# Performance work log

Hardware: AMD Instinct MI355X
Metric: run time of the kernel (lower is better)

Reference implementation:

```python
import jax, jax.numpy as jnp
import numpy as np

N_NODES = 50000
N_EDGES = 800000
NUM_FEATURES = 128
HIDDEN = 64
ODE_STEPS = 32  # fixed-step dopri5 (deterministic stand-in for adaptive dopri5)


def gcn_conv(h, edge_index, W, b):
    """PyG GCNConv: add self-loops, symmetric deg^-1/2 normalization, linear."""
    n = h.shape[0]
    hw = h @ W  # [N, out]
    loops = jnp.arange(n, dtype=edge_index.dtype)
    src = jnp.concatenate([edge_index[0], loops])
    dst = jnp.concatenate([edge_index[1], loops])
    deg = jax.ops.segment_sum(jnp.ones_like(src, dtype=hw.dtype), dst, num_segments=n)
    dinv = jnp.where(deg > 0, jax.lax.rsqrt(deg), 0.0)
    coef = dinv[src] * dinv[dst]  # [E+N]
    msg = hw[src] * coef[:, None]
    out = jax.ops.segment_sum(msg, dst, num_segments=n)
    return out + b


def dopri5_fixed(f, y0, t0, t1, n_steps):
    """Fixed-step Dormand-Prince RK45 from t0 to t1 (autonomous-friendly)."""
    h = (t1 - t0) / n_steps
    A = [
        (1 / 5,),
        (3 / 40, 9 / 40),
        (44 / 45, -56 / 15, 32 / 9),
        (19372 / 6561, -25360 / 2187, 64448 / 6561, -212 / 729),
        (9017 / 3168, -355 / 33, 46732 / 5247, 49 / 176, -5103 / 18656),
        (35 / 384, 0.0, 500 / 1113, 125 / 192, -2187 / 6784, 11 / 84),
    ]
    C = (0.0, 1 / 5, 3 / 10, 4 / 5, 8 / 9, 1.0)
    B = (35 / 384, 0.0, 500 / 1113, 125 / 192, -2187 / 6784, 11 / 84, 0.0)

    def step(y, i):
        t = t0 + h * i.astype(y.dtype)
        ks = [f(t, y)]
        for row, c in zip(A, C[1:]):
            yi = y + h * sum(a * k for a, k in zip(row, ks))
            ks.append(f(t + c * h, yi))
        y_next = y + h * sum(b * k for b, k in zip(B, ks) if b != 0.0)
        return y_next, None

    y, _ = jax.lax.scan(step, y0, jnp.arange(n_steps))
    return y


def setup_inputs() -> dict:
    key = jax.random.key(0)
    ks = jax.random.split(key, 12)
    s = 1.0 / np.sqrt(NUM_FEATURES)
    sh = 1.0 / np.sqrt(HIDDEN)
    s2 = 1.0 / np.sqrt(2 * HIDDEN)
    return {
        "x": jax.random.normal(ks[0], (N_NODES, NUM_FEATURES), jnp.float32),
        "pos_edge_index": jax.random.randint(ks[1], (2, N_EDGES), 0, N_NODES, jnp.int64),
        "neg_edge_index": jax.random.randint(ks[2], (2, N_EDGES), 0, N_NODES, jnp.int64),
        "t": jnp.array([0.0, 1.0], jnp.float32),
        "W_enc": jax.random.uniform(ks[3], (NUM_FEATURES, HIDDEN), jnp.float32, -s, s),
        "b_enc": jax.random.uniform(ks[4], (HIDDEN,), jnp.float32, -s, s),
        "W_pos": jax.random.uniform(ks[5], (HIDDEN, HIDDEN), jnp.float32, -sh, sh),
        "b_pos": jax.random.uniform(ks[6], (HIDDEN,), jnp.float32, -sh, sh),
        "W_neg": jax.random.uniform(ks[7], (HIDDEN, HIDDEN), jnp.float32, -sh, sh),
        "b_neg": jax.random.uniform(ks[8], (HIDDEN,), jnp.float32, -sh, sh),
        "W_ode": jax.random.uniform(ks[9], (2 * HIDDEN, 2 * HIDDEN), jnp.float32, -s2, s2),
        "b_ode": jax.random.uniform(ks[10], (2 * HIDDEN,), jnp.float32, -s2, s2),
    }


def reference(x, pos_edge_index, neg_edge_index, t, W_enc, b_enc, W_pos, b_pos,
              W_neg, b_neg, W_ode, b_ode):
    h = x @ W_enc + b_enc  # feature_encoder
    h_pos = gcn_conv(h, pos_edge_index, W_pos, b_pos)
    h_neg = gcn_conv(h, neg_edge_index, W_neg, b_neg)
    h = jnp.concatenate([h_pos, h_neg], axis=1)  # [N, 2*hidden]

    def ode_f(_t, y):
        return jnp.tanh(y @ W_ode + b_ode)

    return dopri5_fixed(ode_f, h, t[0], t[1], ODE_STEPS)
```

## Files before the change

kernel.cpp:

```cpp
#include <hip/hip_runtime.h>
#include <hip/hip_bf16.h>


typedef __attribute__((ext_vector_type(8))) short short8v;
typedef __attribute__((ext_vector_type(4))) float f32x4;
typedef __attribute__((ext_vector_type(2))) unsigned uint2v;

__device__ __forceinline__ float fast_tanh(float x) {
    float e = __builtin_amdgcn_exp2f(x * 2.8853900817779268f);
    return 1.0f - 2.0f * __builtin_amdgcn_rcpf(e + 1.0f);
}

__device__ __forceinline__ unsigned bf16r(float x) {
    unsigned u = __float_as_uint(x);
    return (u + 0x7fffu + ((u >> 16) & 1u)) >> 16;
}
__device__ __forceinline__ unsigned cvt_pk(float lo, float hi) {
    unsigned r;
    asm("v_cvt_pk_bf16_f32 %0, %1, %2" : "=v"(r) : "v"(lo), "v"(hi));
    return r;
}


__global__ __launch_bounds__(256) void deg_init_kernel(float* degp, float* degn, int n) {
    int i = blockIdx.x * 256 + threadIdx.x;
    if (i < n) { degp[i] = 1.0f; degn[i] = 1.0f; }
}

__global__ __launch_bounds__(256) void deg_count_kernel(const int* __restrict__ pdst,
        const int* __restrict__ ndst, float* degp, float* degn, int nE) {
    int e = blockIdx.x * 256 + threadIdx.x;
    if (e < nE) {
        atomicAdd(&degp[pdst[e]], 1.0f);
        atomicAdd(&degn[ndst[e]], 1.0f);
    }
}

__global__ __launch_bounds__(256) void dinv_kernel(float* degp, float* degn, int n) {
    int i = blockIdx.x * 256 + threadIdx.x;
    if (i < n) { degp[i] = rsqrtf(degp[i]); degn[i] = rsqrtf(degn[i]); }
}


__global__ __launch_bounds__(256) void encoder_kernel(const float* __restrict__ x,
        const float* __restrict__ W, const float* __restrict__ b,
        float* __restrict__ h, int n) {
    __shared__ __align__(16) float Ws[128 * 64];
    __shared__ __align__(16) float xs[4 * 128];
    int tid = threadIdx.x;
    for (int i = tid; i < 128 * 64; i += 256) Ws[i] = W[i];
    long row = (long)blockIdx.x * 4;
    for (int i = tid; i < 4 * 128; i += 256) {
        long rr = row + (i >> 7);
        xs[i] = (rr < n) ? x[rr * 128 + (i & 127)] : 0.0f;
    }
    __syncthreads();
    int r = tid >> 6, c = tid & 63;
    float acc = b[c];
    #pragma unroll 8
    for (int k = 0; k < 128; k += 4) {
        float4 xv = *(const float4*)&xs[r * 128 + k];
        acc += xv.x * Ws[(k+0)*64+c] + xv.y * Ws[(k+1)*64+c]
             + xv.z * Ws[(k+2)*64+c] + xv.w * Ws[(k+3)*64+c];
    }
    if (row + r < n) h[(row + r) * 64 + c] = acc;
}


__global__ __launch_bounds__(256) void hw_kernel(const float* __restrict__ h,
        const float* __restrict__ Wp, const float* __restrict__ Wn,
        const float* __restrict__ dinvp, const float* __restrict__ dinvn,
        float* __restrict__ hwp, float* __restrict__ hwn, int n) {
    __shared__ __align__(16) float Wps[64 * 64];
    __shared__ __align__(16) float Wns[64 * 64];
    __shared__ __align__(16) float hs[4 * 64];
    int tid = threadIdx.x;
    for (int i = tid; i < 64 * 64; i += 256) { Wps[i] = Wp[i]; Wns[i] = Wn[i]; }
    long row = (long)blockIdx.x * 4;
    {
        int i = tid;
        long rr = row + (i >> 6);
        hs[i] = (rr < n) ? h[rr * 64 + (i & 63)] : 0.0f;
    }
    __syncthreads();
    int r = tid >> 6, c = tid & 63;
    float ap = 0.0f, an = 0.0f;
    #pragma unroll 4
    for (int k = 0; k < 64; k += 4) {
        float4 hv = *(const float4*)&hs[r * 64 + k];
        ap += hv.x*Wps[(k+0)*64+c] + hv.y*Wps[(k+1)*64+c] + hv.z*Wps[(k+2)*64+c] + hv.w*Wps[(k+3)*64+c];
        an += hv.x*Wns[(k+0)*64+c] + hv.y*Wns[(k+1)*64+c] + hv.z*Wns[(k+2)*64+c] + hv.w*Wns[(k+3)*64+c];
    }
    if (row + r < n) {
        hwp[(row + r) * 64 + c] = ap * dinvp[row + r];
        hwn[(row + r) * 64 + c] = an * dinvn[row + r];
    }
}


__global__ __launch_bounds__(256) void y0_init_kernel(const float* __restrict__ hwp,
        const float* __restrict__ hwn, float* __restrict__ y0, int n) {
    long idx = (long)blockIdx.x * 256 + threadIdx.x;
    if (idx >= (long)n * 128) return;
    long i = idx >> 7; int c = (int)(idx & 127);
    y0[idx] = (c < 64) ? hwp[i * 64 + c] : hwn[i * 64 + (c - 64)];
}

__global__ __launch_bounds__(256) void scatter_kernel(const int* __restrict__ src,
        const int* __restrict__ dst, const float* __restrict__ hw,
        float* __restrict__ y0, int colOff, int nE) {
    int wid  = blockIdx.x * 4 + (threadIdx.x >> 6);
    int lane = threadIdx.x & 63;
    if (wid >= nE) return;
    int s = src[wid], d = dst[wid];
    atomicAdd(&y0[(long)d * 128 + colOff + lane], hw[(long)s * 64 + lane]);
}

__global__ __launch_bounds__(256) void finalize_kernel(float* __restrict__ y0,
        const float* __restrict__ dinvp, const float* __restrict__ dinvn,
        const float* __restrict__ bp, const float* __restrict__ bn, int n) {
    long idx = (long)blockIdx.x * 256 + threadIdx.x;
    if (idx >= (long)n * 128) return;
    long i = idx >> 7; int c = (int)(idx & 127);
    if (c < 64) y0[idx] = dinvp[i] * y0[idx] + bp[c];
    else        y0[idx] = dinvn[i] * y0[idx] + bn[c - 64];
}


#define MFMA_(A, B, C) __builtin_amdgcn_mfma_f32_16x16x32_bf16(A, B, C, 0, 0, 0)

#define ODE_STAGE(BUF, YIM, CONSM) {                                                \
    char* yr_ = (BUF) + rowoff;                                                     \
    uint2v pk_;                                                                     \
    pk_.x = cvt_pk(YIM(0,0), YIM(0,1)); pk_.y = cvt_pk(YIM(0,2), YIM(0,3));         \
    *(uint2v*)(yr_ + (g0off ^ swz)) = pk_;                                          \
    pk_.x = cvt_pk(YIM(1,0), YIM(1,1)); pk_.y = cvt_pk(YIM(1,2), YIM(1,3));         \
    *(uint2v*)(yr_ + (g1off ^ swz)) = pk_;                                          \
    __syncthreads();                                                                \
    short8v b0 = *(const short8v*)(yr_ + ((  0 + q16) ^ swz));                      \
    short8v b1 = *(const short8v*)(yr_ + (( 64 + q16) ^ swz));                      \
    short8v b2 = *(const short8v*)(yr_ + ((128 + q16) ^ swz));                      \
    short8v b3 = *(const short8v*)(yr_ + ((192 + q16) ^ swz));                      \
    {                                                                               \
        f32x4 a = bias0;                                                            \
        a = MFMA_(af00, b0, a); a = MFMA_(af01, b1, a);                             \
        a = MFMA_(af02, b2, a); a = MFMA_(af03, b3, a);                             \
        CONSM(0, fast_tanh(a[0]), fast_tanh(a[1]), fast_tanh(a[2]), fast_tanh(a[3])); \
    }                                                                               \
    {                                                                               \
        f32x4 a = bias1;                                                            \
        a = MFMA_(af10, b0, a); a = MFMA_(af11, b1, a);                             \
        a = MFMA_(af12, b2, a); a = MFMA_(af13, b3, a);                             \
        CONSM(1, fast_tanh(a[0]), fast_tanh(a[1]), fast_tanh(a[2]), fast_tanh(a[3])); \
    } }

#define YI1(nn, r) (y[nn][r])
#define YI2(nn, r) (y[nn][r] + c21 * kp1[nn][r])
#define YI3(nn, r) (y[nn][r] + c31 * kp1[nn][r] + c32 * kp2[nn][r])
#define YI4(nn, r) (y[nn][r] + c41 * kp1[nn][r] + c42 * kp2[nn][r] + c43 * kp3[nn][r])
#define YI5(nn, r) (y[nn][r] + c51 * kp1[nn][r] + c52 * kp2[nn][r] + c53 * kp3[nn][r] \
                             + c54 * kp4[nn][r])
#define YI6(nn, r) (y[nn][r] + c61 * kp1[nn][r] + c62 * kp2[nn][r] + c63 * kp3[nn][r] \
                             + c64 * kp4[nn][r] + c65 * kp5[nn][r])

#define CONS1(nn,t0,t1,t2,t3) { kp1[nn][0]=t0; kp1[nn][1]=t1; kp1[nn][2]=t2; kp1[nn][3]=t3; }
#define CONS2(nn,t0,t1,t2,t3) { kp2[nn][0]=t0; kp2[nn][1]=t1; kp2[nn][2]=t2; kp2[nn][3]=t3; }
#define CONS3(nn,t0,t1,t2,t3) { kp3[nn][0]=t0; kp3[nn][1]=t1; kp3[nn][2]=t2; kp3[nn][3]=t3; }
#define CONS4(nn,t0,t1,t2,t3) { kp4[nn][0]=t0; kp4[nn][1]=t1; kp4[nn][2]=t2; kp4[nn][3]=t3; }
#define CONS5(nn,t0,t1,t2,t3) { kp5[nn][0]=t0; kp5[nn][1]=t1; kp5[nn][2]=t2; kp5[nn][3]=t3; }
#define CONS6(nn,t0,t1,t2,t3) {                                             \
    y[nn][0] += d1 * kp1[nn][0] + d3 * kp3[nn][0] + d4 * kp4[nn][0]         \
              + d5 * kp5[nn][0] + d6 * (t0);                                \
    y[nn][1] += d1 * kp1[nn][1] + d3 * kp3[nn][1] + d4 * kp4[nn][1]         \
              + d5 * kp5[nn][1] + d6 * (t1);                                \
    y[nn][2] += d1 * kp1[nn][2] + d3 * kp3[nn][2] + d4 * kp4[nn][2]         \
              + d5 * kp5[nn][2] + d6 * (t2);                                \
    y[nn][3] += d1 * kp1[nn][3] + d3 * kp3[nn][3] + d4 * kp4[nn][3]         \
              + d5 * kp5[nn][3] + d6 * (t3); }

__global__ __launch_bounds__(256) void ode_mfma_kernel(const float* __restrict__ y0,
        float* __restrict__ out, const float* __restrict__ W,
        const float* __restrict__ bb, const float* __restrict__ tt, int nrows) {
    __shared__ __align__(16) char smem[32768];
    int tid  = threadIdx.x;
    int lane = tid & 63, w = tid >> 6;
    int l15 = lane & 15, q = lane >> 4;
    int swz = (lane & 7) << 4, q16 = q * 16, q8 = q * 8;
    int rowoff = l15 * 256;
    int g0off = w * 64 + q8, g1off = w * 64 + 32 + q8;

    for (int i = tid; i < 16384; i += 256) {
        int d = i >> 7, c = i & 127;
        unsigned short hb = (unsigned short)bf16r(W[i]);
        *(unsigned short*)(smem + c * 256 + ((d * 2) ^ ((c & 7) << 4))) = hb;
    }
    __syncthreads();

    const char* ab0 = smem + ((2 * w) * 16 + l15) * 256;
    const char* ab1 = smem + ((2 * w + 1) * 16 + l15) * 256;
    short8v af00 = *(const short8v*)(ab0 + ((  0 + q16) ^ swz));
    short8v af01 = *(const short8v*)(ab0 + (( 64 + q16) ^ swz));
    short8v af02 = *(const short8v*)(ab0 + ((128 + q16) ^ swz));
    short8v af03 = *(const short8v*)(ab0 + ((192 + q16) ^ swz));
    short8v af10 = *(const short8v*)(ab1 + ((  0 + q16) ^ swz));
    short8v af11 = *(const short8v*)(ab1 + (( 64 + q16) ^ swz));
    short8v af12 = *(const short8v*)(ab1 + ((128 + q16) ^ swz));
    short8v af13 = *(const short8v*)(ab1 + ((192 + q16) ^ swz));
    __syncthreads();

    float hstep = (tt[1] - tt[0]) * 0.03125f;
    float c21 = hstep * 0.2f;
    float c31 = hstep * 0.075f,               c32 = hstep * 0.225f;
    float c41 = hstep * 0.9777777777777777f,  c42 = hstep * -3.7333333333333334f,
          c43 = hstep * 3.5555555555555554f;
    float c51 = hstep * 2.9525986892242035f,  c52 = hstep * -11.595793324188385f,
          c53 = hstep * 9.822892851699436f,   c54 = hstep * -0.2908093278463649f;
    float c61 = hstep * 2.8462752525252526f,  c62 = hstep * -10.757575757575758f,
          c63 = hstep * 8.906422717743473f,   c64 = hstep * 0.2784090909090909f,
          c65 = hstep * -0.2735313036020583f;
    float d1 = hstep * 0.09114583333333333f,  d3 = hstep * 0.44923629829290207f,
          d4 = hstep * 0.6510416666666666f,   d5 = hstep * -0.322376179245283f,
          d6 = hstep * 0.13095238095238096f;

    f32x4 bias0 = *(const f32x4*)&bb[(2 * w)     * 16 + q * 4];
    f32x4 bias1 = *(const f32x4*)&bb[(2 * w + 1) * 16 + q * 4];

    long grow = (long)blockIdx.x * 16 + l15;
    bool ok = grow < nrows;

    f32x4 y[2];
    if (ok) {
        y[0] = *(const f32x4*)&y0[grow * 128 + (2 * w)     * 16 + q * 4];
        y[1] = *(const f32x4*)&y0[grow * 128 + (2 * w + 1) * 16 + q * 4];
    } else {
        y[0] = (f32x4){0.0f, 0.0f, 0.0f, 0.0f};
        y[1] = (f32x4){0.0f, 0.0f, 0.0f, 0.0f};
    }

    char* bufA = smem;
    char* bufB = smem + 4096;

    f32x4 kp1[2], kp2[2], kp3[2], kp4[2], kp5[2];

    #pragma unroll 1
    for (int step = 0; step < 32; ++step) {
        ODE_STAGE(bufA, YI1, CONS1);
        ODE_STAGE(bufB, YI2, CONS2);
        ODE_STAGE(bufA, YI3, CONS3);
        ODE_STAGE(bufB, YI4, CONS4);
        ODE_STAGE(bufA, YI5, CONS5);
        ODE_STAGE(bufB, YI6, CONS6);
    }

    if (ok) {
        *(f32x4*)&out[grow * 128 + (2 * w)     * 16 + q * 4] = y[0];
        *(f32x4*)&out[grow * 128 + (2 * w + 1) * 16 + q * 4] = y[1];
    }
}


extern "C" void kernel_launch(void* const* d_in, const int* in_sizes, int n_in,
                              void* d_out, int out_size, void* d_ws, size_t ws_size,
                              hipStream_t stream) {
    const float* x     = (const float*)d_in[0];
    const int*   pei   = (const int*)d_in[1];
    const int*   nei   = (const int*)d_in[2];
    const float* t     = (const float*)d_in[3];
    const float* W_enc = (const float*)d_in[4];
    const float* b_enc = (const float*)d_in[5];
    const float* W_pos = (const float*)d_in[6];
    const float* b_pos = (const float*)d_in[7];
    const float* W_neg = (const float*)d_in[8];
    const float* b_neg = (const float*)d_in[9];
    const float* W_ode = (const float*)d_in[10];
    const float* b_ode = (const float*)d_in[11];

    int n  = in_sizes[0] / 128;
    int nE = in_sizes[1] / 2;

    float* ws    = (float*)d_ws;
    float* h     = ws;
    float* y0    = ws + (long)n * 64;
    float* dinvp = y0 + (long)n * 128;
    float* dinvn = dinvp + n;

    float* hwp = (float*)d_out;
    float* hwn = hwp + (long)n * 64;

    const int* psrc = pei;       const int* pdst = pei + nE;
    const int* nsrc = nei;       const int* ndst = nei + nE;

    int nbN  = (n + 255) / 256;
    int nbE  = (nE + 255) / 256;
    int nbR  = (n + 3) / 4;
    long tot = (long)n * 128;
    int nbT  = (int)((tot + 255) / 256);

    deg_init_kernel <<<nbN, 256, 0, stream>>>(dinvp, dinvn, n);
    deg_count_kernel<<<nbE, 256, 0, stream>>>(pdst, ndst, dinvp, dinvn, nE);
    dinv_kernel     <<<nbN, 256, 0, stream>>>(dinvp, dinvn, n);
    encoder_kernel  <<<nbR, 256, 0, stream>>>(x, W_enc, b_enc, h, n);
    hw_kernel       <<<nbR, 256, 0, stream>>>(h, W_pos, W_neg, dinvp, dinvn, hwp, hwn, n);
    y0_init_kernel  <<<nbT, 256, 0, stream>>>(hwp, hwn, y0, n);
    scatter_kernel  <<<(nE + 3) / 4, 256, 0, stream>>>(psrc, pdst, hwp, y0, 0,  nE);
    scatter_kernel  <<<(nE + 3) / 4, 256, 0, stream>>>(nsrc, ndst, hwn, y0, 64, nE);
    finalize_kernel <<<nbT, 256, 0, stream>>>(y0, dinvp, dinvn, b_pos, b_neg, n);
    ode_mfma_kernel <<<(n + 15) / 16, 256, 0, stream>>>(y0, (float*)d_out, W_ode, b_ode, t, n);
}
```

Measured before the change: 1.176 ms.

## Replace atomic scatter with CSR build and per-node gather aggregation

Replaces the float atomicAdd scatter of messages into y0 with a CSR build (count, single-block scan, fill) and a gather kernel where one wavefront per destination node sums neighbour rows. The degree normalization, self-loop and bias are folded into the gather, which removes the y0_init and finalize passes. The goal is to avoid roughly 100M float atomics and the extra full passes over y0. In exchange it adds integer atomics for counting and filling, plus a serial-ish 2-block scan over 50k nodes. The workspace formerly used for h is reused for the CSR arrays after hw_kernel has consumed h.

```diff
diff --git a/kernel.cpp b/kernel.cpp
--- a/kernel.cpp
+++ b/kernel.cpp
@@ -19,26 +19,6 @@
     unsigned r;
     asm("v_cvt_pk_bf16_f32 %0, %1, %2" : "=v"(r) : "v"(lo), "v"(hi));
     return r;
-}
-
-
-__global__ __launch_bounds__(256) void deg_init_kernel(float* degp, float* degn, int n) {
-    int i = blockIdx.x * 256 + threadIdx.x;
-    if (i < n) { degp[i] = 1.0f; degn[i] = 1.0f; }
-}
-
-__global__ __launch_bounds__(256) void deg_count_kernel(const int* __restrict__ pdst,
-        const int* __restrict__ ndst, float* degp, float* degn, int nE) {
-    int e = blockIdx.x * 256 + threadIdx.x;
-    if (e < nE) {
-        atomicAdd(&degp[pdst[e]], 1.0f);
-        atomicAdd(&degn[ndst[e]], 1.0f);
-    }
-}
-
-__global__ __launch_bounds__(256) void dinv_kernel(float* degp, float* degn, int n) {
-    int i = blockIdx.x * 256 + threadIdx.x;
-    if (i < n) { degp[i] = rsqrtf(degp[i]); degn[i] = rsqrtf(degn[i]); }
 }
 
 
@@ -69,7 +49,6 @@
 
 __global__ __launch_bounds__(256) void hw_kernel(const float* __restrict__ h,
         const float* __restrict__ Wp, const float* __restrict__ Wn,
-        const float* __restrict__ dinvp, const float* __restrict__ dinvn,
         float* __restrict__ hwp, float* __restrict__ hwn, int n) {
     __shared__ __align__(16) float Wps[64 * 64];
     __shared__ __align__(16) float Wns[64 * 64];
@@ -92,38 +71,114 @@
         an += hv.x*Wns[(k+0)*64+c] + hv.y*Wns[(k+1)*64+c] + hv.z*Wns[(k+2)*64+c] + hv.w*Wns[(k+3)*64+c];
     }
     if (row + r < n) {
-        hwp[(row + r) * 64 + c] = ap * dinvp[row + r];
-        hwn[(row + r) * 64 + c] = an * dinvn[row + r];
-    }
-}
-
-
-__global__ __launch_bounds__(256) void y0_init_kernel(const float* __restrict__ hwp,
-        const float* __restrict__ hwn, float* __restrict__ y0, int n) {
-    long idx = (long)blockIdx.x * 256 + threadIdx.x;
-    if (idx >= (long)n * 128) return;
-    long i = idx >> 7; int c = (int)(idx & 127);
-    y0[idx] = (c < 64) ? hwp[i * 64 + c] : hwn[i * 64 + (c - 64)];
-}
-
-__global__ __launch_bounds__(256) void scatter_kernel(const int* __restrict__ src,
-        const int* __restrict__ dst, const float* __restrict__ hw,
-        float* __restrict__ y0, int colOff, int nE) {
-    int wid  = blockIdx.x * 4 + (threadIdx.x >> 6);
-    int lane = threadIdx.x & 63;
-    if (wid >= nE) return;
-    int s = src[wid], d = dst[wid];
-    atomicAdd(&y0[(long)d * 128 + colOff + lane], hw[(long)s * 64 + lane]);
-}
-
-__global__ __launch_bounds__(256) void finalize_kernel(float* __restrict__ y0,
+        hwp[(row + r) * 64 + c] = ap;
+        hwn[(row + r) * 64 + c] = an;
+    }
+}
+
+
+__global__ __launch_bounds__(256) void cnt_zero_kernel(int* cntp, int* cntn, int n) {
+    int i = blockIdx.x * 256 + threadIdx.x;
+    if (i < n) { cntp[i] = 0; cntn[i] = 0; }
+}
+
+__global__ __launch_bounds__(256) void count_kernel(const int* __restrict__ pdst,
+        const int* __restrict__ ndst, int* cntp, int* cntn, int nE) {
+    int e = blockIdx.x * 256 + threadIdx.x;
+    if (e < nE) {
+        atomicAdd(&cntp[pdst[e]], 1);
+        atomicAdd(&cntn[ndst[e]], 1);
+    }
+}
+
+__global__ __launch_bounds__(1024) void scan_kernel(int* cntp, int* cntn,
+        int* rpp, int* rpn, float* dinvp, float* dinvn, int n) {
+    int* cnt  = blockIdx.x ? cntn  : cntp;
+    int* rp   = blockIdx.x ? rpn   : rpp;
+    float* dv = blockIdx.x ? dinvn : dinvp;
+    __shared__ int ps[1024];
+    int t = threadIdx.x;
+    int CH = (n + 1023) / 1024;
+    int beg = t * CH, end = beg + CH; if (end > n) end = n;
+    int s = 0;
+    for (int i = beg; i < end && i >= 0; ++i) s += cnt[i];
+    ps[t] = s;
+    __syncthreads();
+    for (int off = 1; off < 1024; off <<= 1) {
+        int v = (t >= off) ? ps[t - off] : 0;
+        __syncthreads();
+        ps[t] += v;
+        __syncthreads();
+    }
+    int run = (t == 0) ? 0 : ps[t - 1];
+    for (int i = beg; i < end && i >= 0; ++i) {
+        int c = cnt[i];
+        rp[i] = run; run += c;
+        dv[i] = rsqrtf((float)c + 1.0f);
+        cnt[i] = 0;
+    }
+    if (t == 1023) rp[n] = ps[1023];
+}
+
+__global__ __launch_bounds__(256) void fill_kernel(const int* __restrict__ src,
+        const int* __restrict__ dst, const int* __restrict__ rp,
+        int* cur, int* outarr, int nE) {
+    int e = blockIdx.x * 256 + threadIdx.x;
+    if (e >= nE) return;
+    int d = dst[e];
+    int pos = rp[d] + atomicAdd(&cur[d], 1);
+    outarr[pos] = src[e];
+}
+
+
+__global__ __launch_bounds__(256) void aggregate_kernel(
+        const float* __restrict__ hwp, const float* __restrict__ hwn,
+        const int* __restrict__ srcp, const int* __restrict__ srcn,
+        const int* __restrict__ rpp, const int* __restrict__ rpn,
         const float* __restrict__ dinvp, const float* __restrict__ dinvn,
-        const float* __restrict__ bp, const float* __restrict__ bn, int n) {
-    long idx = (long)blockIdx.x * 256 + threadIdx.x;
-    if (idx >= (long)n * 128) return;
-    long i = idx >> 7; int c = (int)(idx & 127);
-    if (c < 64) y0[idx] = dinvp[i] * y0[idx] + bp[c];
-    else        y0[idx] = dinvn[i] * y0[idx] + bn[c - 64];
+        const float* __restrict__ bp, const float* __restrict__ bn,
+        float* __restrict__ y0, int n) {
+    int w = threadIdx.x >> 6, lane = threadIdx.x & 63;
+    int d = blockIdx.x * 4 + w;
+    if (d >= n) return;
+    {
+        int beg = rpp[d], end = rpp[d + 1];
+        float s0 = 0, s1 = 0, s2 = 0, s3 = 0;
+        int i = beg;
+        for (; i + 4 <= end; i += 4) {
+            int a0 = srcp[i], a1 = srcp[i+1], a2 = srcp[i+2], a3 = srcp[i+3];
+            s0 += dinvp[a0] * hwp[(long)a0 * 64 + lane];
+            s1 += dinvp[a1] * hwp[(long)a1 * 64 + lane];
+            s2 += dinvp[a2] * hwp[(long)a2 * 64 + lane];
+            s3 += dinvp[a3] * hwp[(long)a3 * 64 + lane];
+        }
+        for (; i < end; ++i) {
+            int a0 = srcp[i];
+            s0 += dinvp[a0] * hwp[(long)a0 * 64 + lane];
+        }
+        float dv = dinvp[d];
+        float sum = (s0 + s1) + (s2 + s3) + dv * hwp[(long)d * 64 + lane];
+        y0[(long)d * 128 + lane] = dv * sum + bp[lane];
+    }
+    {
+        int beg = rpn[d], end = rpn[d + 1];
+        float s0 = 0, s1 = 0, s2 = 0, s3 = 0;
+        int i = beg;
+        for (; i + 4 <= end; i += 4) {
+            int a0 = srcn[i], a1 = srcn[i+1], a2 = srcn[i+2], a3 = srcn[i+3];
+            s0 += dinvn[a0] * hwn[(long)a0 * 64 + lane];
+            s1 += dinvn[a1] * hwn[(long)a1 * 64 + lane];
+            s2 += dinvn[a2] * hwn[(long)a2 * 64 + lane];
+            s3 += dinvn[a3] * hwn[(long)a3 * 64 + lane];
+        }
+        for (; i < end; ++i) {
+            int a0 = srcn[i];
+            s0 += dinvn[a0] * hwn[(long)a0 * 64 + lane];
+        }
+        float dv = dinvn[d];
+        float sum = (s0 + s1) + (s2 + s3) + dv * hwn[(long)d * 64 + lane];
+        y0[(long)d * 128 + 64 + lane] = dv * sum + bn[lane];
+    }
 }
 
 
@@ -284,26 +339,32 @@
     float* dinvp = y0 + (long)n * 128;
     float* dinvn = dinvp + n;
 
+    int* csr  = (int*)h;
+    int* srcp = csr;
+    int* srcn = srcp + nE;
+    int* cntp = srcn + nE;
+    int* cntn = cntp + n;
+    int* rpp  = cntn + n;
+    int* rpn  = rpp + (n + 1);
+
     float* hwp = (float*)d_out;
     float* hwn = hwp + (long)n * 64;
 
     const int* psrc = pei;       const int* pdst = pei + nE;
     const int* nsrc = nei;       const int* ndst = nei + nE;
 
-    int nbN  = (n + 255) / 256;
-    int nbE  = (nE + 255) / 256;
-    int nbR  = (n + 3) / 4;
-    long tot = (long)n * 128;
-    int nbT  = (int)((tot + 255) / 256);
-
-    deg_init_kernel <<<nbN, 256, 0, stream>>>(dinvp, dinvn, n);
-    deg_count_kernel<<<nbE, 256, 0, stream>>>(pdst, ndst, dinvp, dinvn, nE);
-    dinv_kernel     <<<nbN, 256, 0, stream>>>(dinvp, dinvn, n);
+    int nbN = (n + 255) / 256;
+    int nbE = (nE + 255) / 256;
+    int nbR = (n + 3) / 4;
+
     encoder_kernel  <<<nbR, 256, 0, stream>>>(x, W_enc, b_enc, h, n);
-    hw_kernel       <<<nbR, 256, 0, stream>>>(h, W_pos, W_neg, dinvp, dinvn, hwp, hwn, n);
-    y0_init_kernel  <<<nbT, 256, 0, stream>>>(hwp, hwn, y0, n);
-    scatter_kernel  <<<(nE + 3) / 4, 256, 0, stream>>>(psrc, pdst, hwp, y0, 0,  nE);
-    scatter_kernel  <<<(nE + 3) / 4, 256, 0, stream>>>(nsrc, ndst, hwn, y0, 64, nE);
-    finalize_kernel <<<nbT, 256, 0, stream>>>(y0, dinvp, dinvn, b_pos, b_neg, n);
+    hw_kernel       <<<nbR, 256, 0, stream>>>(h, W_pos, W_neg, hwp, hwn, n);
+    cnt_zero_kernel <<<nbN, 256, 0, stream>>>(cntp, cntn, n);
+    count_kernel    <<<nbE, 256, 0, stream>>>(pdst, ndst, cntp, cntn, nE);
+    scan_kernel     <<<2, 1024, 0, stream>>>(cntp, cntn, rpp, rpn, dinvp, dinvn, n);
+    fill_kernel     <<<nbE, 256, 0, stream>>>(psrc, pdst, rpp, cntp, srcp, nE);
+    fill_kernel     <<<nbE, 256, 0, stream>>>(nsrc, ndst, rpn, cntn, srcn, nE);
+    aggregate_kernel<<<nbR, 256, 0, stream>>>(hwp, hwn, srcp, srcn, rpp, rpn,
+                                              dinvp, dinvn, b_pos, b_neg, y0, n);
     ode_mfma_kernel <<<(n + 15) / 16, 256, 0, stream>>>(y0, (float*)d_out, W_ode, b_ode, t, n);
 }
```

New measurement: 1.074 ms. -8.6%, faster.
